# Kernel tuning notes

Hardware: AMD Instinct MI355X
Metric: run time of the kernel (lower is better)

Reference implementation:

```python
import jax, jax.numpy as jnp
import numpy as np

B, S, IN, OUT = 4, 2048, 4096, 11008


def setup_inputs() -> dict:
    key = jax.random.key(0)
    k1, k2, k3, k4 = jax.random.split(key, 4)
    x = jax.random.normal(k1, (B, S, IN), dtype=jnp.float32)
    # int8 weight codes (stored as int32 for portability; values in [0,127))
    weight_int8 = jax.random.randint(k2, (OUT, IN), 0, 127, dtype=jnp.int32)
    scale = jax.random.uniform(k3, (OUT,), dtype=jnp.float32) * 0.01 + 1e-4
    bias = jax.random.normal(k4, (OUT,), dtype=jnp.float32)
    return {"x": x, "weight_int8": weight_int8, "scale": scale, "bias": bias}


def reference(x, weight_int8, scale, bias):
    # dequantize: int8 codes -> fp, per-output-row scale (scale.view(-1,1) in torch)
    w = weight_int8.astype(jnp.float32) * scale[:, None]  # [OUT, IN]
    # F.linear(x, w, bias) == x @ w.T + bias
    out = jnp.einsum('bsi,oi->bso', x, w) + bias  # [B, S, OUT]
    return out
```

## Files before the change

kernel.cpp:

```cpp
#include <hip/hip_runtime.h>
#include <hip/hip_bf16.h>
#include <stdint.h>


#define MT 8192
#define KT 4096
#define NT 11008
#define NKT 32
#define MTILES 32
#define NTILES 43
#define CHUNK_BYTES 32768

typedef __attribute__((ext_vector_type(8))) short short8;
typedef __attribute__((ext_vector_type(4))) float f32x4;
typedef __attribute__((ext_vector_type(4))) int i32x4;
typedef __attribute__((ext_vector_type(16))) int i32x16;
typedef __attribute__((ext_vector_type(16))) char char16;

static __device__ __forceinline__ short f2bf(float f) {
  union { float f; unsigned u; } c; c.f = f;
  unsigned u = c.u;
  return (short)((u + 0x7fffu + ((u >> 16) & 1u)) >> 16);
}

__global__ __launch_bounds__(256) void quant_x_kernel(const float* __restrict__ in,
                                                      char* __restrict__ Aws,
                                                      float* __restrict__ sx) {
  const int m = blockIdx.x;
  const int t = threadIdx.x;
  const float* row = in + (size_t)m * KT + t * 16;
  f32x4 v[4];
  float mx = 0.f;
#pragma unroll
  for (int i = 0; i < 4; i++) {
    v[i] = *(const f32x4*)(row + i * 4);
#pragma unroll
    for (int j = 0; j < 4; j++) mx = fmaxf(mx, fabsf(v[i][j]));
  }
#pragma unroll
  for (int off = 32; off; off >>= 1) mx = fmaxf(mx, __shfl_xor(mx, off));
  __shared__ float smx[4];
  if ((t & 63) == 0) smx[t >> 6] = mx;
  __syncthreads();
  mx = fmaxf(fmaxf(smx[0], smx[1]), fmaxf(smx[2], smx[3]));
  const float inv = 127.0f / mx;
  if (t == 0) sx[m] = mx * (1.0f / 127.0f);
  char16 q;
#pragma unroll
  for (int i = 0; i < 4; i++)
#pragma unroll
    for (int j = 0; j < 4; j++) q[i * 4 + j] = (char)(int)rintf(v[i][j] * inv);
  const int mt = m >> 8, r = m & 255, kt = t >> 3, g = t & 7;
  *(char16*)(Aws + ((size_t)mt * NKT + kt) * CHUNK_BYTES + r * 128 +
             ((g * 16) ^ ((r & 7) << 4))) = q;
}

__global__ __launch_bounds__(256) void cvt_w8_kernel(const int* __restrict__ in,
                                                     char* __restrict__ Bws) {
  const int n = blockIdx.x;
  const int t = threadIdx.x;
  const int* s = in + (size_t)n * KT + t * 16;
  char16 q;
#pragma unroll
  for (int i = 0; i < 4; i++) {
    i32x4 a = *(const i32x4*)(s + i * 4);
#pragma unroll
    for (int j = 0; j < 4; j++) q[i * 4 + j] = (char)a[j];
  }
  const int nt = n >> 8, r = n & 255, kt = t >> 3, g = t & 7;
  *(char16*)(Bws + ((size_t)nt * NKT + kt) * CHUNK_BYTES + r * 128 +
             ((g * 16) ^ ((r & 7) << 4))) = q;
}


#define GLD(chunk, j, ldsbase)                                                   \
  __builtin_amdgcn_global_load_lds(                                              \
      (const __attribute__((address_space(1))) void*)((chunk) + (j) * 4096 +     \
                                                      tid * 16),                 \
      (__attribute__((address_space(3))) void*)((ldsbase) + (j) * 4096 +         \
                                                wid * 1024),                     \
      16, 0, 0)

#define GLDALL(Achunk, Bchunk, dA, dB)                                         \
  do {                                                                         \
    GLD(Bchunk, 0, dB); GLD(Bchunk, 1, dB); GLD(Bchunk, 2, dB);                \
    GLD(Bchunk, 3, dB); GLD(Bchunk, 4, dB); GLD(Bchunk, 5, dB);                \
    GLD(Bchunk, 6, dB); GLD(Bchunk, 7, dB);                                    \
    GLD(Achunk, 0, dA); GLD(Achunk, 1, dA); GLD(Achunk, 2, dA);                \
    GLD(Achunk, 3, dA); GLD(Achunk, 4, dA); GLD(Achunk, 5, dA);                \
    GLD(Achunk, 6, dA); GLD(Achunk, 7, dA);                                    \
  } while (0)

#define BAR asm volatile("s_barrier" ::: "memory")
#define VMC0 asm volatile("s_waitcnt vmcnt(0)" ::: "memory")

#define KOFF(s) ((((s) * 32) + khalf) ^ swz)

#define LDSL(LAp, s, aset, bset)                             \
  do {                                                       \
    const int ko_ = KOFF(s);                                 \
    aset[0] = *(const i32x4*)((LAp) + aoff + ko_);           \
    aset[1] = *(const i32x4*)((LAp) + aoff + 4096 + ko_);    \
    aset[2] = *(const i32x4*)((LAp) + aoff + 8192 + ko_);    \
    aset[3] = *(const i32x4*)((LAp) + aoff + 12288 + ko_);   \
    bset[0] = *(const i32x4*)((LAp) + boff + ko_);           \
    bset[1] = *(const i32x4*)((LAp) + boff + 4096 + ko_);    \
    bset[2] = *(const i32x4*)((LAp) + boff + 8192 + ko_);    \
    bset[3] = *(const i32x4*)((LAp) + boff + 12288 + ko_);   \
  } while (0)

#define MMS(aset, bset)                                                        \
  do {                                                                         \
    __builtin_amdgcn_s_setprio(1);                                             \
    _Pragma("unroll") for (int mb = 0; mb < 4; mb++)                           \
        _Pragma("unroll") for (int nb = 0; nb < 4; nb++)                       \
            acc[mb][nb] = __builtin_amdgcn_mfma_i32_32x32x32_i8(               \
                aset[mb], bset[nb], acc[mb][nb], 0, 0, 0);                     \
    __builtin_amdgcn_s_setprio(0);                                             \
  } while (0)

__global__ __launch_bounds__(256, 1) void gemm256(
    const char* __restrict__ Aws, const char* __restrict__ Bws,
    const float* __restrict__ sx, const float* __restrict__ scale,
    const float* __restrict__ bias, float* __restrict__ out) {
  extern __shared__ char Lsm[];
  const int tid = threadIdx.x;
  const int lane = tid & 63;
  const int wid = tid >> 6;
  const int wr = wid >> 1;
  const int wc = wid & 1;

  const int bid = blockIdx.x;
  const int lid = (bid & 7) * 172 + (bid >> 3);
  const int g8 = lid / 344;
  const int r8 = lid - g8 * 344;
  const int mt = g8 * 8 + (r8 & 7);
  const int nt = r8 >> 3;

  const char* Ach = Aws + (size_t)mt * NKT * CHUNK_BYTES;
  const char* Bch = Bws + (size_t)nt * NKT * CHUNK_BYTES;

  const int aoff = (wr * 128 + (lane & 31)) * 128;
  const int boff = 32768 + (wc * 128 + (lane & 31)) * 128;
  const int khalf = (lane >> 5) * 16;
  const int swz = (lane & 7) << 4;

  i32x16 acc[4][4] = {};
  i32x4 a0[4], a1[4], b0[4], b1[4];

  {
    GLDALL(Ach, Bch, Lsm, Lsm + 32768);
    VMC0;
    BAR;
    const char* A1 = Ach + CHUNK_BYTES;
    const char* B1 = Bch + CHUNK_BYTES;
    GLDALL(A1, B1, Lsm + 65536, Lsm + 65536 + 32768);
    LDSL(Lsm, 0, a0, b0);
  }

  for (int t = 0; t < NKT; ++t) {
    const char* LA = Lsm + (t & 1) * 65536;

    LDSL(LA, 1, a1, b1);  MMS(a0, b0);
    LDSL(LA, 2, a0, b0);  MMS(a1, b1);
    LDSL(LA, 3, a1, b1);  MMS(a0, b0);
    MMS(a1, b1);

    VMC0;
    BAR;

    if (t + 1 < NKT) {
      const char* LAn = Lsm + ((t + 1) & 1) * 65536;
      LDSL(LAn, 0, a0, b0);
      if (t + 2 < NKT) {
        char* dA = Lsm + (t & 1) * 65536;
        GLDALL(Ach + 2 * CHUNK_BYTES, Bch + 2 * CHUNK_BYTES, dA, dA + 32768);
      }
    }
    Ach += CHUNK_BYTES;
    Bch += CHUNK_BYTES;
  }

  const int col0 = nt * 256 + wc * 128 + (lane & 31);
  const int row0 = mt * 256 + wr * 128 + ((lane >> 5) << 2);
#pragma unroll
  for (int mb = 0; mb < 4; mb++) {
    f32x4 sxq[4];
#pragma unroll
    for (int g = 0; g < 4; g++)
      sxq[g] = *(const f32x4*)(sx + row0 + mb * 32 + g * 8);
#pragma unroll
    for (int nb = 0; nb < 4; nb++) {
      const int n = col0 + nb * 32;
      const float sc = scale[n];
      const float bs = bias[n];
#pragma unroll
      for (int g = 0; g < 4; g++)
#pragma unroll
        for (int j = 0; j < 4; j++) {
          const int row = row0 + mb * 32 + g * 8 + j;
          out[(size_t)row * NT + n] =
              (float)acc[mb][nb][g * 4 + j] * (sxq[g][j] * sc) + bs;
        }
    }
  }
}

__global__ __launch_bounds__(256) void gemm_fallback(
    const float* __restrict__ Ap, const int* __restrict__ Bp,
    const float* __restrict__ scale, const float* __restrict__ bias,
    float* __restrict__ out) {
  __shared__ short ldsA[128 * 64];
  __shared__ short ldsB[128 * 64];
  const int tid = threadIdx.x;
  const int lane = tid & 63;
  const int wid = tid >> 6;
  const int nbn = NT / 128;
  const int cpx = ((MT / 128) * nbn) / 8;
  const int bid = blockIdx.x;
  const int wg = (bid & 7) * cpx + (bid >> 3);
  const int brow = (wg / nbn) * 128;
  const int bcol = (wg % nbn) * 128;
  const int wr = wid >> 1, wc = wid & 1;
  f32x4 acc[4][4] = {{{0.f, 0.f, 0.f, 0.f}}};
  const int srow = tid >> 3;
  const int sk8 = (tid & 7) * 8;
  for (int k0 = 0; k0 < KT; k0 += 64) {
    __syncthreads();
#pragma unroll
    for (int p = 0; p < 4; p++) {
      const int row = p * 32 + srow;
      const float* s = Ap + (size_t)(brow + row) * KT + k0 + sk8;
      f32x4 lo = *(const f32x4*)s;
      f32x4 hi = *(const f32x4*)(s + 4);
      short8 v;
#pragma unroll
      for (int j = 0; j < 4; j++) { v[j] = f2bf(lo[j]); v[4 + j] = f2bf(hi[j]); }
      int bo = (row * 64 + sk8) * 2;
      bo ^= ((row & 7) << 4);
      *(short8*)((char*)ldsA + bo) = v;
    }
#pragma unroll
    for (int p = 0; p < 4; p++) {
      const int row = p * 32 + srow;
      const int* s = Bp + (size_t)(bcol + row) * KT + k0 + sk8;
      i32x4 lo = *(const i32x4*)(s);
      i32x4 hi = *(const i32x4*)(s + 4);
      short8 v;
#pragma unroll
      for (int j = 0; j < 4; j++) { v[j] = f2bf((float)lo[j]); v[4 + j] = f2bf((float)hi[j]); }
      int bo = (row * 64 + sk8) * 2;
      bo ^= ((row & 7) << 4);
      *(short8*)((char*)ldsB + bo) = v;
    }
    __syncthreads();
#pragma unroll
    for (int kk = 0; kk < 2; kk++) {
      short8 af[4], bf2[4];
#pragma unroll
      for (int mi = 0; mi < 4; mi++) {
        const int row = wr * 64 + mi * 16 + (lane & 15);
        int bo = (row * 64 + kk * 32 + (lane >> 4) * 8) * 2;
        bo ^= ((row & 7) << 4);
        af[mi] = *(const short8*)((const char*)ldsA + bo);
      }
#pragma unroll
      for (int ni = 0; ni < 4; ni++) {
        const int row = wc * 64 + ni * 16 + (lane & 15);
        int bo = (row * 64 + kk * 32 + (lane >> 4) * 8) * 2;
        bo ^= ((row & 7) << 4);
        bf2[ni] = *(const short8*)((const char*)ldsB + bo);
      }
#pragma unroll
      for (int mi = 0; mi < 4; mi++)
#pragma unroll
        for (int ni = 0; ni < 4; ni++)
          acc[mi][ni] = __builtin_amdgcn_mfma_f32_16x16x32_bf16(af[mi], bf2[ni],
                                                                acc[mi][ni], 0, 0, 0);
    }
  }
#pragma unroll
  for (int ni = 0; ni < 4; ni++) {
    const int n = bcol + wc * 64 + ni * 16 + (lane & 15);
    const float sc = scale[n];
    const float bs = bias[n];
#pragma unroll
    for (int mi = 0; mi < 4; mi++) {
      const int m0 = brow + wr * 64 + mi * 16 + ((lane >> 4) << 2);
#pragma unroll
      for (int j = 0; j < 4; j++)
        out[(size_t)(m0 + j) * NT + n] = acc[mi][ni][j] * sc + bs;
    }
  }
}

extern "C" void kernel_launch(void* const* d_in, const int* in_sizes, int n_in,
                              void* d_out, int out_size, void* d_ws, size_t ws_size,
                              hipStream_t stream) {
  const float* x = (const float*)d_in[0];
  const int* w = (const int*)d_in[1];
  const float* scale = (const float*)d_in[2];
  const float* bias = (const float*)d_in[3];
  float* out = (float*)d_out;

  const size_t a_bytes = (size_t)MTILES * NKT * CHUNK_BYTES;
  const size_t b_bytes = (size_t)NTILES * NKT * CHUNK_BYTES;
  const size_t s_bytes = (size_t)MT * sizeof(float);

  if (ws_size >= a_bytes + b_bytes + s_bytes) {
    char* aw = (char*)d_ws;
    char* bw = aw + a_bytes;
    float* sx = (float*)(bw + b_bytes);
    quant_x_kernel<<<dim3(MT), dim3(256), 0, stream>>>(x, aw, sx);
    cvt_w8_kernel<<<dim3(NT), dim3(256), 0, stream>>>(w, bw);
    hipFuncSetAttribute((const void*)gemm256,
                        hipFuncAttributeMaxDynamicSharedMemorySize, 131072);
    gemm256<<<dim3(MTILES * NTILES), dim3(256), 131072, stream>>>(
        aw, bw, sx, scale, bias, out);
  } else {
    gemm_fallback<<<dim3((MT / 128) * (NT / 128)), dim3(256), 0, stream>>>(
        x, w, scale, bias, out);
  }
}
```

Baseline: 525.1 us.

## Shrink GEMM tile to 128x128 with 16x16x64 int8 MFMA and two blocks per CU

Changes the int8 GEMM tile from 256x256 to 128x128 output and switches the MFMA from 32x32x32 to 16x16x64 int8. The workspace chunk layout changes to match, and the block swizzle is remapped. LDS use drops to 64KB so two blocks can share a CU, and the grid grows to 5504 blocks. The intent is better occupancy and latency hiding, paid for with half the operand reuse per tile and twice the global/LDS traffic per FLOP.

```diff
diff --git a/kernel.cpp b/kernel.cpp
--- a/kernel.cpp
+++ b/kernel.cpp
@@ -7,14 +7,13 @@
 #define KT 4096
 #define NT 11008
 #define NKT 32
-#define MTILES 32
-#define NTILES 43
-#define CHUNK_BYTES 32768
+#define MTILES 64
+#define NTILES 86
+#define CHUNK_BYTES 16384
 
 typedef __attribute__((ext_vector_type(8))) short short8;
 typedef __attribute__((ext_vector_type(4))) float f32x4;
 typedef __attribute__((ext_vector_type(4))) int i32x4;
-typedef __attribute__((ext_vector_type(16))) int i32x16;
 typedef __attribute__((ext_vector_type(16))) char char16;
 
 static __device__ __forceinline__ short f2bf(float f) {
@@ -50,7 +49,7 @@
   for (int i = 0; i < 4; i++)
 #pragma unroll
     for (int j = 0; j < 4; j++) q[i * 4 + j] = (char)(int)rintf(v[i][j] * inv);
-  const int mt = m >> 8, r = m & 255, kt = t >> 3, g = t & 7;
+  const int mt = m >> 7, r = m & 127, kt = t >> 3, g = t & 7;
   *(char16*)(Aws + ((size_t)mt * NKT + kt) * CHUNK_BYTES + r * 128 +
              ((g * 16) ^ ((r & 7) << 4))) = q;
 }
@@ -67,7 +66,7 @@
 #pragma unroll
     for (int j = 0; j < 4; j++) q[i * 4 + j] = (char)a[j];
   }
-  const int nt = n >> 8, r = n & 255, kt = t >> 3, g = t & 7;
+  const int nt = n >> 7, r = n & 127, kt = t >> 3, g = t & 7;
   *(char16*)(Bws + ((size_t)nt * NKT + kt) * CHUNK_BYTES + r * 128 +
              ((g * 16) ^ ((r & 7) << 4))) = q;
 }
@@ -81,45 +80,43 @@
                                                 wid * 1024),                     \
       16, 0, 0)
 
-#define GLDALL(Achunk, Bchunk, dA, dB)                                         \
-  do {                                                                         \
-    GLD(Bchunk, 0, dB); GLD(Bchunk, 1, dB); GLD(Bchunk, 2, dB);                \
-    GLD(Bchunk, 3, dB); GLD(Bchunk, 4, dB); GLD(Bchunk, 5, dB);                \
-    GLD(Bchunk, 6, dB); GLD(Bchunk, 7, dB);                                    \
-    GLD(Achunk, 0, dA); GLD(Achunk, 1, dA); GLD(Achunk, 2, dA);                \
-    GLD(Achunk, 3, dA); GLD(Achunk, 4, dA); GLD(Achunk, 5, dA);                \
-    GLD(Achunk, 6, dA); GLD(Achunk, 7, dA);                                    \
+#define GLDALL(Achunk, Bchunk, dA, dB)                          \
+  do {                                                          \
+    GLD(Bchunk, 0, dB); GLD(Bchunk, 1, dB);                     \
+    GLD(Bchunk, 2, dB); GLD(Bchunk, 3, dB);                     \
+    GLD(Achunk, 0, dA); GLD(Achunk, 1, dA);                     \
+    GLD(Achunk, 2, dA); GLD(Achunk, 3, dA);                     \
   } while (0)
 
 #define BAR asm volatile("s_barrier" ::: "memory")
 #define VMC0 asm volatile("s_waitcnt vmcnt(0)" ::: "memory")
 
-#define KOFF(s) ((((s) * 32) + khalf) ^ swz)
+#define KOFF(s) ((((s) * 64) + khalf) ^ swz)
 
 #define LDSL(LAp, s, aset, bset)                             \
   do {                                                       \
     const int ko_ = KOFF(s);                                 \
     aset[0] = *(const i32x4*)((LAp) + aoff + ko_);           \
-    aset[1] = *(const i32x4*)((LAp) + aoff + 4096 + ko_);    \
-    aset[2] = *(const i32x4*)((LAp) + aoff + 8192 + ko_);    \
-    aset[3] = *(const i32x4*)((LAp) + aoff + 12288 + ko_);   \
+    aset[1] = *(const i32x4*)((LAp) + aoff + 2048 + ko_);    \
+    aset[2] = *(const i32x4*)((LAp) + aoff + 4096 + ko_);    \
+    aset[3] = *(const i32x4*)((LAp) + aoff + 6144 + ko_);    \
     bset[0] = *(const i32x4*)((LAp) + boff + ko_);           \
-    bset[1] = *(const i32x4*)((LAp) + boff + 4096 + ko_);    \
-    bset[2] = *(const i32x4*)((LAp) + boff + 8192 + ko_);    \
-    bset[3] = *(const i32x4*)((LAp) + boff + 12288 + ko_);   \
+    bset[1] = *(const i32x4*)((LAp) + boff + 2048 + ko_);    \
+    bset[2] = *(const i32x4*)((LAp) + boff + 4096 + ko_);    \
+    bset[3] = *(const i32x4*)((LAp) + boff + 6144 + ko_);    \
   } while (0)
 
 #define MMS(aset, bset)                                                        \
   do {                                                                         \
     __builtin_amdgcn_s_setprio(1);                                             \
-    _Pragma("unroll") for (int mb = 0; mb < 4; mb++)                           \
-        _Pragma("unroll") for (int nb = 0; nb < 4; nb++)                       \
-            acc[mb][nb] = __builtin_amdgcn_mfma_i32_32x32x32_i8(               \
-                aset[mb], bset[nb], acc[mb][nb], 0, 0, 0);                     \
+    _Pragma("unroll") for (int mi = 0; mi < 4; mi++)                           \
+        _Pragma("unroll") for (int ni = 0; ni < 4; ni++)                       \
+            acc[mi][ni] = __builtin_amdgcn_mfma_i32_16x16x64_i8(               \
+                aset[mi], bset[ni], acc[mi][ni], 0, 0, 0);                     \
     __builtin_amdgcn_s_setprio(0);                                             \
   } while (0)
 
-__global__ __launch_bounds__(256, 1) void gemm256(
+__global__ __launch_bounds__(256, 2) void gemm128(
     const char* __restrict__ Aws, const char* __restrict__ Bws,
     const float* __restrict__ sx, const float* __restrict__ scale,
     const float* __restrict__ bias, float* __restrict__ out) {
@@ -131,77 +128,70 @@
   const int wc = wid & 1;
 
   const int bid = blockIdx.x;
-  const int lid = (bid & 7) * 172 + (bid >> 3);
-  const int g8 = lid / 344;
-  const int r8 = lid - g8 * 344;
+  const int lid = (bid & 7) * 688 + (bid >> 3);
+  const int g8 = lid / 688;
+  const int r8 = lid - g8 * 688;
   const int mt = g8 * 8 + (r8 & 7);
   const int nt = r8 >> 3;
 
   const char* Ach = Aws + (size_t)mt * NKT * CHUNK_BYTES;
   const char* Bch = Bws + (size_t)nt * NKT * CHUNK_BYTES;
 
-  const int aoff = (wr * 128 + (lane & 31)) * 128;
-  const int boff = 32768 + (wc * 128 + (lane & 31)) * 128;
-  const int khalf = (lane >> 5) * 16;
+  const int aoff = (wr * 64 + (lane & 15)) * 128;
+  const int boff = 16384 + (wc * 64 + (lane & 15)) * 128;
+  const int khalf = (lane >> 4) * 16;
   const int swz = (lane & 7) << 4;
 
-  i32x16 acc[4][4] = {};
+  i32x4 acc[4][4] = {};
   i32x4 a0[4], a1[4], b0[4], b1[4];
 
   {
-    GLDALL(Ach, Bch, Lsm, Lsm + 32768);
+    GLDALL(Ach, Bch, Lsm, Lsm + 16384);
     VMC0;
     BAR;
     const char* A1 = Ach + CHUNK_BYTES;
     const char* B1 = Bch + CHUNK_BYTES;
-    GLDALL(A1, B1, Lsm + 65536, Lsm + 65536 + 32768);
+    GLDALL(A1, B1, Lsm + 32768, Lsm + 32768 + 16384);
     LDSL(Lsm, 0, a0, b0);
   }
 
   for (int t = 0; t < NKT; ++t) {
-    const char* LA = Lsm + (t & 1) * 65536;
-
-    LDSL(LA, 1, a1, b1);  MMS(a0, b0);
-    LDSL(LA, 2, a0, b0);  MMS(a1, b1);
-    LDSL(LA, 3, a1, b1);  MMS(a0, b0);
+    const char* LA = Lsm + (t & 1) * 32768;
+
+    LDSL(LA, 1, a1, b1);
+    MMS(a0, b0);
     MMS(a1, b1);
 
     VMC0;
     BAR;
 
     if (t + 1 < NKT) {
-      const char* LAn = Lsm + ((t + 1) & 1) * 65536;
+      const char* LAn = Lsm + ((t + 1) & 1) * 32768;
       LDSL(LAn, 0, a0, b0);
       if (t + 2 < NKT) {
-        char* dA = Lsm + (t & 1) * 65536;
-        GLDALL(Ach + 2 * CHUNK_BYTES, Bch + 2 * CHUNK_BYTES, dA, dA + 32768);
+        char* dA = Lsm + (t & 1) * 32768;
+        GLDALL(Ach + 2 * CHUNK_BYTES, Bch + 2 * CHUNK_BYTES, dA, dA + 16384);
       }
     }
     Ach += CHUNK_BYTES;
     Bch += CHUNK_BYTES;
   }
 
-  const int col0 = nt * 256 + wc * 128 + (lane & 31);
-  const int row0 = mt * 256 + wr * 128 + ((lane >> 5) << 2);
-#pragma unroll
-  for (int mb = 0; mb < 4; mb++) {
-    f32x4 sxq[4];
-#pragma unroll
-    for (int g = 0; g < 4; g++)
-      sxq[g] = *(const f32x4*)(sx + row0 + mb * 32 + g * 8);
-#pragma unroll
-    for (int nb = 0; nb < 4; nb++) {
-      const int n = col0 + nb * 32;
+  const int col0 = nt * 128 + wc * 64 + (lane & 15);
+  const int row0 = mt * 128 + wr * 64 + ((lane >> 4) << 2);
+#pragma unroll
+  for (int mi = 0; mi < 4; mi++) {
+    const f32x4 sxq = *(const f32x4*)(sx + row0 + mi * 16);
+#pragma unroll
+    for (int ni = 0; ni < 4; ni++) {
+      const int n = col0 + ni * 16;
       const float sc = scale[n];
       const float bs = bias[n];
 #pragma unroll
-      for (int g = 0; g < 4; g++)
-#pragma unroll
-        for (int j = 0; j < 4; j++) {
-          const int row = row0 + mb * 32 + g * 8 + j;
-          out[(size_t)row * NT + n] =
-              (float)acc[mb][nb][g * 4 + j] * (sxq[g][j] * sc) + bs;
-        }
+      for (int j = 0; j < 4; j++) {
+        const int row = row0 + mi * 16 + j;
+        out[(size_t)row * NT + n] = (float)acc[mi][ni][j] * (sxq[j] * sc) + bs;
+      }
     }
   }
 }
@@ -313,9 +303,9 @@
     float* sx = (float*)(bw + b_bytes);
     quant_x_kernel<<<dim3(MT), dim3(256), 0, stream>>>(x, aw, sx);
     cvt_w8_kernel<<<dim3(NT), dim3(256), 0, stream>>>(w, bw);
-    hipFuncSetAttribute((const void*)gemm256,
-                        hipFuncAttributeMaxDynamicSharedMemorySize, 131072);
-    gemm256<<<dim3(MTILES * NTILES), dim3(256), 131072, stream>>>(
+    hipFuncSetAttribute((const void*)gemm128,
+                        hipFuncAttributeMaxDynamicSharedMemorySize, 65536);
+    gemm128<<<dim3(MTILES * NTILES), dim3(256), 65536, stream>>>(
         aw, bw, sx, scale, bias, out);
   } else {
     gemm_fallback<<<dim3((MT / 128) * (NT / 128)), dim3(256), 0, stream>>>(
```

Result: faster. 497.1 us (-5.3%).

## Load B fragments directly to registers, shrink N tile to 128, two blocks per CU

Applied to the files above, without the earlier changes.

Changes the int8 GEMM from 256x256 tiles with A and B both staged in LDS to 256x128 tiles where only A goes through LDS. Each wave loads its B fragments straight from global memory into registers in an MFMA-ready layout, prefetching one k-step ahead. The quantize and convert kernels are rewritten to emit this pre-permuted fragment layout, and LDS use is halved so two blocks can share a CU. The intent is to remove B's LDS traffic and raise occupancy, at the cost of reloading A twice as often and issuing more global loads per wave.

```diff
diff --git a/kernel.cpp b/kernel.cpp
--- a/kernel.cpp
+++ b/kernel.cpp
@@ -8,8 +8,9 @@
 #define NT 11008
 #define NKT 32
 #define MTILES 32
-#define NTILES 43
-#define CHUNK_BYTES 32768
+#define NTILES 86
+#define CHUNK_A 32768
+#define CHUNK_B 16384
 
 typedef __attribute__((ext_vector_type(8))) short short8;
 typedef __attribute__((ext_vector_type(4))) float f32x4;
@@ -50,26 +51,30 @@
   for (int i = 0; i < 4; i++)
 #pragma unroll
     for (int j = 0; j < 4; j++) q[i * 4 + j] = (char)(int)rintf(v[i][j] * inv);
-  const int mt = m >> 8, r = m & 255, kt = t >> 3, g = t & 7;
-  *(char16*)(Aws + ((size_t)mt * NKT + kt) * CHUNK_BYTES + r * 128 +
-             ((g * 16) ^ ((r & 7) << 4))) = q;
+  const int kt = t >> 3, s = (t >> 1) & 3, hi = t & 1;
+  const int lane = (m & 31) | (hi << 5);
+  const int r32 = (m >> 5) & 7;
+  *(char16*)(Aws + ((size_t)(m >> 8) * NKT + kt) * CHUNK_A +
+             (r32 * 4 + s) * 1024 + lane * 16) = q;
 }
 
 __global__ __launch_bounds__(256) void cvt_w8_kernel(const int* __restrict__ in,
                                                      char* __restrict__ Bws) {
   const int n = blockIdx.x;
   const int t = threadIdx.x;
-  const int* s = in + (size_t)n * KT + t * 16;
+  const int* s_ = in + (size_t)n * KT + t * 16;
   char16 q;
 #pragma unroll
   for (int i = 0; i < 4; i++) {
-    i32x4 a = *(const i32x4*)(s + i * 4);
+    i32x4 a = *(const i32x4*)(s_ + i * 4);
 #pragma unroll
     for (int j = 0; j < 4; j++) q[i * 4 + j] = (char)a[j];
   }
-  const int nt = n >> 8, r = n & 255, kt = t >> 3, g = t & 7;
-  *(char16*)(Bws + ((size_t)nt * NKT + kt) * CHUNK_BYTES + r * 128 +
-             ((g * 16) ^ ((r & 7) << 4))) = q;
+  const int kt = t >> 3, s = (t >> 1) & 3, hi = t & 1;
+  const int lane = (n & 31) | (hi << 5);
+  const int c32 = (n >> 5) & 3;
+  *(char16*)(Bws + ((size_t)(n >> 7) * NKT + kt) * CHUNK_B +
+             (c32 * 4 + s) * 1024 + lane * 16) = q;
 }
 
 
@@ -81,45 +86,76 @@
                                                 wid * 1024),                     \
       16, 0, 0)
 
-#define GLDALL(Achunk, Bchunk, dA, dB)                                         \
-  do {                                                                         \
-    GLD(Bchunk, 0, dB); GLD(Bchunk, 1, dB); GLD(Bchunk, 2, dB);                \
-    GLD(Bchunk, 3, dB); GLD(Bchunk, 4, dB); GLD(Bchunk, 5, dB);                \
-    GLD(Bchunk, 6, dB); GLD(Bchunk, 7, dB);                                    \
-    GLD(Achunk, 0, dA); GLD(Achunk, 1, dA); GLD(Achunk, 2, dA);                \
-    GLD(Achunk, 3, dA); GLD(Achunk, 4, dA); GLD(Achunk, 5, dA);                \
-    GLD(Achunk, 6, dA); GLD(Achunk, 7, dA);                                    \
+#define GLDA(chunk, dst)                                       \
+  do {                                                         \
+    GLD(chunk, 0, dst); GLD(chunk, 1, dst);                    \
+    GLD(chunk, 2, dst); GLD(chunk, 3, dst);                    \
+    GLD(chunk, 4, dst); GLD(chunk, 5, dst);                    \
+    GLD(chunk, 6, dst); GLD(chunk, 7, dst);                    \
   } while (0)
 
 #define BAR asm volatile("s_barrier" ::: "memory")
 #define VMC0 asm volatile("s_waitcnt vmcnt(0)" ::: "memory")
 
-#define KOFF(s) ((((s) * 32) + khalf) ^ swz)
-
-#define LDSL(LAp, s, aset, bset)                             \
-  do {                                                       \
-    const int ko_ = KOFF(s);                                 \
-    aset[0] = *(const i32x4*)((LAp) + aoff + ko_);           \
-    aset[1] = *(const i32x4*)((LAp) + aoff + 4096 + ko_);    \
-    aset[2] = *(const i32x4*)((LAp) + aoff + 8192 + ko_);    \
-    aset[3] = *(const i32x4*)((LAp) + aoff + 12288 + ko_);   \
-    bset[0] = *(const i32x4*)((LAp) + boff + ko_);           \
-    bset[1] = *(const i32x4*)((LAp) + boff + 4096 + ko_);    \
-    bset[2] = *(const i32x4*)((LAp) + boff + 8192 + ko_);    \
-    bset[3] = *(const i32x4*)((LAp) + boff + 12288 + ko_);   \
+#define LOADB(B_, src)                                         \
+  do {                                                         \
+    const char* bb_ = (src) + wc * 8192 + lane * 16;           \
+    B_[0][0] = *(const i32x4*)(bb_);                           \
+    B_[0][1] = *(const i32x4*)(bb_ + 1024);                    \
+    B_[0][2] = *(const i32x4*)(bb_ + 2048);                    \
+    B_[0][3] = *(const i32x4*)(bb_ + 3072);                    \
+    B_[1][0] = *(const i32x4*)(bb_ + 4096);                    \
+    B_[1][1] = *(const i32x4*)(bb_ + 5120);                    \
+    B_[1][2] = *(const i32x4*)(bb_ + 6144);                    \
+    B_[1][3] = *(const i32x4*)(bb_ + 7168);                    \
   } while (0)
 
-#define MMS(aset, bset)                                                        \
+#define LDSL(LAp, s, aset)                                     \
+  do {                                                         \
+    const char* a_ = (LAp) + albase + (s) * 1024;              \
+    aset[0] = *(const i32x4*)(a_);                             \
+    aset[1] = *(const i32x4*)(a_ + 4096);                      \
+    aset[2] = *(const i32x4*)(a_ + 8192);                      \
+    aset[3] = *(const i32x4*)(a_ + 12288);                     \
+  } while (0)
+
+#define MMS(aset, BC, s)                                                       \
   do {                                                                         \
     __builtin_amdgcn_s_setprio(1);                                             \
     _Pragma("unroll") for (int mb = 0; mb < 4; mb++)                           \
-        _Pragma("unroll") for (int nb = 0; nb < 4; nb++)                       \
+        _Pragma("unroll") for (int nb = 0; nb < 2; nb++)                       \
             acc[mb][nb] = __builtin_amdgcn_mfma_i32_32x32x32_i8(               \
-                aset[mb], bset[nb], acc[mb][nb], 0, 0, 0);                     \
+                aset[mb], BC[nb][s], acc[mb][nb], 0, 0, 0);                    \
     __builtin_amdgcn_s_setprio(0);                                             \
   } while (0)
 
-__global__ __launch_bounds__(256, 1) void gemm256(
+#define TILE_BODY(BC, BN_)                                                     \
+  {                                                                            \
+    const char* LA = Lsm + (t & 1) * 32768;                                    \
+    if (t + 1 < NKT) LOADB(BN_, Bch + CHUNK_B);                                \
+    LDSL(LA, 1, a1);                                                           \
+    MMS(a0, BC, 0);                                                            \
+    LDSL(LA, 2, a0);                                                           \
+    MMS(a1, BC, 1);                                                            \
+    LDSL(LA, 3, a1);                                                           \
+    MMS(a0, BC, 2);                                                            \
+    MMS(a1, BC, 3);                                                            \
+    VMC0;                                                                      \
+    BAR;                                                                       \
+    if (t + 1 < NKT) {                                                         \
+      const char* LAn = Lsm + ((t + 1) & 1) * 32768;                           \
+      LDSL(LAn, 0, a0);                                                        \
+      if (t + 2 < NKT) {                                                       \
+        char* dA = Lsm + (t & 1) * 32768;                                      \
+        GLDA(Ach + 2 * CHUNK_A, dA);                                           \
+      }                                                                        \
+    }                                                                          \
+    Ach += CHUNK_A;                                                            \
+    Bch += CHUNK_B;                                                            \
+    ++t;                                                                       \
+  }
+
+__global__ __launch_bounds__(256, 2) void gemm_bless(
     const char* __restrict__ Aws, const char* __restrict__ Bws,
     const float* __restrict__ sx, const float* __restrict__ scale,
     const float* __restrict__ bias, float* __restrict__ out) {
@@ -131,57 +167,33 @@
   const int wc = wid & 1;
 
   const int bid = blockIdx.x;
-  const int lid = (bid & 7) * 172 + (bid >> 3);
-  const int g8 = lid / 344;
-  const int r8 = lid - g8 * 344;
-  const int mt = g8 * 8 + (r8 & 7);
-  const int nt = r8 >> 3;
-
-  const char* Ach = Aws + (size_t)mt * NKT * CHUNK_BYTES;
-  const char* Bch = Bws + (size_t)nt * NKT * CHUNK_BYTES;
-
-  const int aoff = (wr * 128 + (lane & 31)) * 128;
-  const int boff = 32768 + (wc * 128 + (lane & 31)) * 128;
-  const int khalf = (lane >> 5) * 16;
-  const int swz = (lane & 7) << 4;
-
-  i32x16 acc[4][4] = {};
-  i32x4 a0[4], a1[4], b0[4], b1[4];
+  const int r = bid >> 3;
+  const int mt = (bid & 7) * 4 + (r & 3);
+  const int nt = r >> 2;
+
+  const char* Ach = Aws + (size_t)mt * NKT * CHUNK_A;
+  const char* Bch = Bws + (size_t)nt * NKT * CHUNK_B;
+
+  const int albase = wr * 16384 + lane * 16;
+
+  i32x16 acc[4][2] = {};
+  i32x4 a0[4], a1[4], bA[2][4], bB[2][4];
 
   {
-    GLDALL(Ach, Bch, Lsm, Lsm + 32768);
+    GLDA(Ach, Lsm);
+    LOADB(bA, Bch);
     VMC0;
     BAR;
-    const char* A1 = Ach + CHUNK_BYTES;
-    const char* B1 = Bch + CHUNK_BYTES;
-    GLDALL(A1, B1, Lsm + 65536, Lsm + 65536 + 32768);
-    LDSL(Lsm, 0, a0, b0);
-  }
-
-  for (int t = 0; t < NKT; ++t) {
-    const char* LA = Lsm + (t & 1) * 65536;
-
-    LDSL(LA, 1, a1, b1);  MMS(a0, b0);
-    LDSL(LA, 2, a0, b0);  MMS(a1, b1);
-    LDSL(LA, 3, a1, b1);  MMS(a0, b0);
-    MMS(a1, b1);
-
-    VMC0;
-    BAR;
-
-    if (t + 1 < NKT) {
-      const char* LAn = Lsm + ((t + 1) & 1) * 65536;
-      LDSL(LAn, 0, a0, b0);
-      if (t + 2 < NKT) {
-        char* dA = Lsm + (t & 1) * 65536;
-        GLDALL(Ach + 2 * CHUNK_BYTES, Bch + 2 * CHUNK_BYTES, dA, dA + 32768);
-      }
-    }
-    Ach += CHUNK_BYTES;
-    Bch += CHUNK_BYTES;
-  }
-
-  const int col0 = nt * 256 + wc * 128 + (lane & 31);
+    GLDA(Ach + CHUNK_A, Lsm + 32768);
+    LDSL(Lsm, 0, a0);
+  }
+
+  for (int t = 0; t < NKT;) {
+    TILE_BODY(bA, bB);
+    TILE_BODY(bB, bA);
+  }
+
+  const int col_base = nt * 128 + wc * 64 + (lane & 31);
   const int row0 = mt * 256 + wr * 128 + ((lane >> 5) << 2);
 #pragma unroll
   for (int mb = 0; mb < 4; mb++) {
@@ -190,8 +202,8 @@
     for (int g = 0; g < 4; g++)
       sxq[g] = *(const f32x4*)(sx + row0 + mb * 32 + g * 8);
 #pragma unroll
-    for (int nb = 0; nb < 4; nb++) {
-      const int n = col0 + nb * 32;
+    for (int nb = 0; nb < 2; nb++) {
+      const int n = col_base + nb * 32;
       const float sc = scale[n];
       const float bs = bias[n];
 #pragma unroll
@@ -303,8 +315,8 @@
   const float* bias = (const float*)d_in[3];
   float* out = (float*)d_out;
 
-  const size_t a_bytes = (size_t)MTILES * NKT * CHUNK_BYTES;
-  const size_t b_bytes = (size_t)NTILES * NKT * CHUNK_BYTES;
+  const size_t a_bytes = (size_t)MTILES * NKT * CHUNK_A;
+  const size_t b_bytes = (size_t)NTILES * NKT * CHUNK_B;
   const size_t s_bytes = (size_t)MT * sizeof(float);
 
   if (ws_size >= a_bytes + b_bytes + s_bytes) {
@@ -313,9 +325,9 @@
     float* sx = (float*)(bw + b_bytes);
     quant_x_kernel<<<dim3(MT), dim3(256), 0, stream>>>(x, aw, sx);
     cvt_w8_kernel<<<dim3(NT), dim3(256), 0, stream>>>(w, bw);
-    hipFuncSetAttribute((const void*)gemm256,
-                        hipFuncAttributeMaxDynamicSharedMemorySize, 131072);
-    gemm256<<<dim3(MTILES * NTILES), dim3(256), 131072, stream>>>(
+    hipFuncSetAttribute((const void*)gemm_bless,
+                        hipFuncAttributeMaxDynamicSharedMemorySize, 65536);
+    gemm_bless<<<dim3(MTILES * NTILES), dim3(256), 65536, stream>>>(
         aw, bw, sx, scale, bias, out);
   } else {
     gemm_fallback<<<dim3((MT / 128) * (NT / 128)), dim3(256), 0, stream>>>(
```

After: 521.5 us. No clear change (-0.7%).
